# Optimization experiments

Hardware: AMD Instinct MI355X
Metric: run time of the kernel (lower is better)

## Reference

```python
import jax, jax.numpy as jnp
import numpy as np

N0 = 100000
N1 = 100000
K = 16
D_MODEL = 64
D_ATTN = 32
H = 4


def setup_inputs() -> dict:
    key = jax.random.key(0)
    ks = jax.random.split(key, 12)
    inp = {
        "coords0": jax.random.normal(ks[0], (N0, 3), jnp.float32),
        "coords1": jax.random.normal(ks[1], (N1, 3), jnp.float32),
        "feats0": jax.random.normal(ks[2], (N0, D_MODEL), jnp.float32),
        "feats1": jax.random.normal(ks[3], (N1, D_MODEL), jnp.float32),
        "knn_idxs": jax.random.randint(ks[4], (1, N1, K), 0, N0, jnp.int64 if jax.config.jax_enable_x64 else jnp.int32),
        # Linear params (PyTorch Linear: y = x @ W.T + b; stored here already transposed as [in, out])
        "Wq": jax.random.normal(ks[5], (D_MODEL, D_ATTN), jnp.float32) / np.sqrt(D_MODEL),
        "bq": jnp.zeros((D_ATTN,), jnp.float32),
        "Wk": jax.random.normal(ks[6], (D_MODEL + 3, D_ATTN), jnp.float32) / np.sqrt(D_MODEL + 3),
        "bk": jnp.zeros((D_ATTN,), jnp.float32),
        "Wv": jax.random.normal(ks[7], (D_MODEL + 3, D_MODEL), jnp.float32) / np.sqrt(D_MODEL + 3),
        "bv": jnp.zeros((D_MODEL,), jnp.float32),
    }
    return inp


def reference(coords0, coords1, feats0, feats1, knn_idxs, Wq, bq, Wk, bk, Wv, bv):
    idx = knn_idxs[0]  # [N1, K] neighbor indices into cloud 0
    n1, k_ = idx.shape
    dh_attn = D_ATTN // H   # per-head query/key depth
    dh_val = D_MODEL // H   # per-head value depth

    # Irregular gathers from source cloud
    g_feats = feats0[idx]                         # [N1, K, D_MODEL]
    rel = coords0[idx] - coords1[:, None, :]      # [N1, K, 3] relative coords
    kv_in = jnp.concatenate([g_feats, rel], axis=-1)  # [N1, K, D_MODEL+3]

    # Projections + head split
    q = (feats1 @ Wq + bq).reshape(n1, H, dh_attn)                    # [N1, H, dh]
    k = (kv_in @ Wk + bk).reshape(n1, k_, H, dh_attn).transpose(0, 2, 1, 3)  # [N1, H, K, dh]
    v = (kv_in @ Wv + bv).reshape(n1, k_, H, dh_val).transpose(0, 2, 1, 3)   # [N1, H, K, dv]

    # Attention over K neighbors per point
    attn = jnp.einsum('nhd,nhkd->nhk', q, k) / np.sqrt(dh_attn).astype(np.float32)
    attn = jax.nn.softmax(attn, axis=-1)          # [N1, H, K]
    out = jnp.einsum('nhk,nhkd->nhd', attn, v)    # [N1, H, dv]
    out = out.reshape(n1, -1)                     # [N1, D_MODEL]
    return out, knn_idxs
```

## Files before the change

kernel.cpp:

```cpp
#include <hip/hip_runtime.h>


using half8   = __attribute__((ext_vector_type(8))) _Float16;
using floatx4 = __attribute__((ext_vector_type(4))) float;

template<int CTRL>
__device__ __forceinline__ float dppAdd(float x) {
    int y = __builtin_amdgcn_update_dpp(0, __float_as_int(x), CTRL, 0xF, 0xF, true);
    return x + __int_as_float(y);
}
__device__ __forceinline__ float rowSum16(float x) {
    x = dppAdd<0x121>(x);
    x = dppAdd<0x122>(x);
    x = dppAdd<0x124>(x);
    x = dppAdd<0x128>(x);
    return x;
}

__global__ __launch_bounds__(256, 4) void proj_fused(
    const float* __restrict__ coords0,
    const float* __restrict__ feats0, const float* __restrict__ feats1,
    const float* __restrict__ Wq, const float* __restrict__ bq,
    const float* __restrict__ Wk, const float* __restrict__ bk,
    const float* __restrict__ Wv, const float* __restrict__ bv,
    _Float16* __restrict__ KVh, float* __restrict__ Qf,
    int n0, int n1, int nb0)
{
    __shared__ __align__(16) _Float16 sFrag[6144];
    __shared__ __align__(16) _Float16 sOut[6656];

    const int tid  = threadIdx.x;
    const int wave = tid >> 6;
    const int lane = tid & 63;
    const int l15  = lane & 15;
    const int quad = lane >> 4;

    if ((int)blockIdx.x < nb0) {
        const int rowBase = blockIdx.x * 64;
        for (int e = tid; e < 6144; e += 256) {
            int j = e & 7, ln = (e >> 3) & 63, h = (e >> 9) & 1, t = e >> 10;
            int k = h * 32 + ((ln >> 4) * 8) + j;
            int n = t * 16 + (ln & 15);
            float v = (n < 32) ? Wk[k * 32 + n] : Wv[k * 64 + (n - 32)];
            sFrag[e] = (_Float16)v;
        }
        __syncthreads();

        const int m0   = rowBase + wave * 16;
        const int row  = m0 + l15;
        const int rowc = (row < n0) ? row : (n0 - 1);
        const floatx4* X4 = (const floatx4*)(feats0 + (size_t)rowc * 64);
        floatx4 f0 = X4[quad * 2 + 0], f1 = X4[quad * 2 + 1];
        floatx4 f2 = X4[quad * 2 + 8], f3 = X4[quad * 2 + 9];
        half8 a0, a1;
        a0[0]=(_Float16)f0.x; a0[1]=(_Float16)f0.y; a0[2]=(_Float16)f0.z; a0[3]=(_Float16)f0.w;
        a0[4]=(_Float16)f1.x; a0[5]=(_Float16)f1.y; a0[6]=(_Float16)f1.z; a0[7]=(_Float16)f1.w;
        a1[0]=(_Float16)f2.x; a1[1]=(_Float16)f2.y; a1[2]=(_Float16)f2.z; a1[3]=(_Float16)f2.w;
        a1[4]=(_Float16)f3.x; a1[5]=(_Float16)f3.y; a1[6]=(_Float16)f3.z; a1[7]=(_Float16)f3.w;

        const half8* bf = (const half8*)sFrag;
        floatx4 acc[6];
        #pragma unroll
        for (int t = 0; t < 6; t++) {
            int n = t * 16 + l15;
            float bb = (n < 32) ? bk[n] : bv[n - 32];
            acc[t] = (floatx4){bb, bb, bb, bb};
        }
        #pragma unroll
        for (int t = 0; t < 6; t++) {
            acc[t] = __builtin_amdgcn_mfma_f32_16x16x32_f16(a0, bf[(t*2+0)*64 + lane], acc[t], 0,0,0);
            acc[t] = __builtin_amdgcn_mfma_f32_16x16x32_f16(a1, bf[(t*2+1)*64 + lane], acc[t], 0,0,0);
        }

        #pragma unroll
        for (int t = 0; t < 6; t++)
            #pragma unroll
            for (int r = 0; r < 4; r++)
                sOut[(wave * 16 + quad * 4 + r) * 104 + t * 16 + l15] = (_Float16)acc[t][r];

        for (int r2 = tid; r2 < 64; r2 += 256) {
            int rr = rowBase + r2;
            int rc = (rr < n0) ? rr : (n0 - 1);
            float* cw = (float*)(sOut + r2 * 104 + 96);
            cw[0] = coords0[(size_t)rc * 3 + 0];
            cw[1] = coords0[(size_t)rc * 3 + 1];
            cw[2] = coords0[(size_t)rc * 3 + 2];
            cw[3] = 0.f;
        }
        __syncthreads();

        const half8* so8 = (const half8*)sOut;
        half8* dst = (half8*)(KVh + (size_t)rowBase * 104);
        for (int c = tid; c < 832; c += 256) {
            int r = c / 13;
            if (rowBase + r < n0) dst[c] = so8[c];
        }
    } else {
        const int rowBase = ((int)blockIdx.x - nb0) * 64;
        for (int e = tid; e < 2048; e += 256) {
            int j = e & 7, ln = (e >> 3) & 63, h = (e >> 9) & 1, t = e >> 10;
            int k = h * 32 + ((ln >> 4) * 8) + j;
            int n = t * 16 + (ln & 15);
            sFrag[e] = (_Float16)Wq[k * 32 + n];
        }
        __syncthreads();

        const int m0   = rowBase + wave * 16;
        const int row  = m0 + l15;
        const int rowc = (row < n1) ? row : (n1 - 1);
        const floatx4* X4 = (const floatx4*)(feats1 + (size_t)rowc * 64);
        floatx4 f0 = X4[quad * 2 + 0], f1 = X4[quad * 2 + 1];
        floatx4 f2 = X4[quad * 2 + 8], f3 = X4[quad * 2 + 9];
        half8 a0, a1;
        a0[0]=(_Float16)f0.x; a0[1]=(_Float16)f0.y; a0[2]=(_Float16)f0.z; a0[3]=(_Float16)f0.w;
        a0[4]=(_Float16)f1.x; a0[5]=(_Float16)f1.y; a0[6]=(_Float16)f1.z; a0[7]=(_Float16)f1.w;
        a1[0]=(_Float16)f2.x; a1[1]=(_Float16)f2.y; a1[2]=(_Float16)f2.z; a1[3]=(_Float16)f2.w;
        a1[4]=(_Float16)f3.x; a1[5]=(_Float16)f3.y; a1[6]=(_Float16)f3.z; a1[7]=(_Float16)f3.w;

        const half8* bf = (const half8*)sFrag;
        floatx4 acc[2];
        #pragma unroll
        for (int t = 0; t < 2; t++) {
            float bb = bq[t * 16 + l15];
            acc[t] = (floatx4){bb, bb, bb, bb};
        }
        #pragma unroll
        for (int t = 0; t < 2; t++) {
            acc[t] = __builtin_amdgcn_mfma_f32_16x16x32_f16(a0, bf[(t*2+0)*64 + lane], acc[t], 0,0,0);
            acc[t] = __builtin_amdgcn_mfma_f32_16x16x32_f16(a1, bf[(t*2+1)*64 + lane], acc[t], 0,0,0);
        }
        #pragma unroll
        for (int t = 0; t < 2; t++)
            #pragma unroll
            for (int r = 0; r < 4; r++) {
                int ro = m0 + quad * 4 + r;
                if (ro < n1) Qf[(size_t)ro * 32 + t * 16 + l15] = acc[t][r];
            }
    }
}

__global__ __launch_bounds__(256, 4) void attn_kernel(
    const float* __restrict__ coords1,
    const int*   __restrict__ knn,
    const float* __restrict__ Qf, const _Float16* __restrict__ KVh,
    const float* __restrict__ Wk, const float* __restrict__ Wv,
    float* __restrict__ out, float* __restrict__ outIdx, int n1)
{
    __shared__ __align__(16) float sQ[16][36];
    __shared__ float sWk3[3][32];
    __shared__ float sWv3[3][64];
    __shared__ __align__(16) float sT[16][12];
    __shared__ __align__(16) int   sIdx[16][16];
    __shared__ __align__(16) float sA[16][68];

    const int tid = threadIdx.x;
    for (int e = tid; e < 288; e += 256) {
        if (e < 96) ((float*)sWk3)[e] = Wk[2048 + e];
        else        ((float*)sWv3)[e - 96] = Wv[4096 + (e - 96)];
    }
    if (tid < 128) {
        int pt = tid >> 3, c4 = tid & 7;
        int r = blockIdx.x * 16 + pt;
        if (r >= n1) r = n1 - 1;
        ((floatx4*)&sQ[pt][0])[c4] = ((const floatx4*)Qf)[(size_t)r * 8 + c4];
    }
    __syncthreads();

    const int p = tid >> 4;
    const int j = tid & 15;
    const int n = blockIdx.x * 16 + p;
    const bool valid = (n < n1);
    const int nc = valid ? n : (n1 - 1);

    const int idx = knn[nc * 16 + j];

    const half8* kr = (const half8*)(KVh + (size_t)idx * 104);
    half8 k8_0 = kr[0], k8_1 = kr[1], k8_2 = kr[2], k8_3 = kr[3];
    floatx4 cg = *(const floatx4*)(KVh + (size_t)idx * 104 + 96);

    const float r0 = cg[0] - coords1[nc * 3 + 0];
    const float r1 = cg[1] - coords1[nc * 3 + 1];
    const float r2 = cg[2] - coords1[nc * 3 + 2];

    const int g    = j & 7;
    const int hf   = j >> 3;
    const int h    = g >> 1;
    const int slot = ((j & 1) << 3) + (j >> 1);

    sIdx[p][slot] = idx;

    if (j < 12) {
        int c = j >> 2, h2 = j & 3;
        float t = 0.f;
        #pragma unroll
        for (int i = 0; i < 8; i++)
            t = fmaf(sWk3[c][h2 * 8 + i], sQ[p][h2 * 8 + i], t);
        sT[p][j] = t;
    }

    const int4* si4 = (const int4*)&sIdx[p][hf * 8];
    int4 viA = si4[0], viB = si4[1];
    int vIdx[8] = {viA.x, viA.y, viA.z, viA.w, viB.x, viB.y, viB.z, viB.w};
    half8 v8[8];
    #pragma unroll
    for (int s = 0; s < 8; s++)
        v8[s] = *(const half8*)(KVh + (size_t)vIdx[s] * 104 + 32 + g * 8);

    const floatx4* t4 = (const floatx4*)&sT[p][0];
    floatx4 tc0 = t4[0], tc1 = t4[1], tc2 = t4[2];

    const float scale = 0.35355339059327373f;
    float a_h[4];
    {
        half8 k8[4] = {k8_0, k8_1, k8_2, k8_3};
        #pragma unroll
        for (int h2 = 0; h2 < 4; h2++) {
            floatx4 q0 = ((const floatx4*)&sQ[p][0])[h2 * 2 + 0];
            floatx4 q1 = ((const floatx4*)&sQ[p][0])[h2 * 2 + 1];
            float acc = r0 * tc0[h2] + r1 * tc1[h2] + r2 * tc2[h2];
            acc = fmaf(q0[0], (float)k8[h2][0], acc);
            acc = fmaf(q0[1], (float)k8[h2][1], acc);
            acc = fmaf(q0[2], (float)k8[h2][2], acc);
            acc = fmaf(q0[3], (float)k8[h2][3], acc);
            acc = fmaf(q1[0], (float)k8[h2][4], acc);
            acc = fmaf(q1[1], (float)k8[h2][5], acc);
            acc = fmaf(q1[2], (float)k8[h2][6], acc);
            acc = fmaf(q1[3], (float)k8[h2][7], acc);
            float e = __expf(acc * scale);
            float ssum = rowSum16(e);
            a_h[h2] = e * __builtin_amdgcn_rcpf(ssum);
        }
    }

    sA[p][0 * 16 + slot] = a_h[0];
    sA[p][1 * 16 + slot] = a_h[1];
    sA[p][2 * 16 + slot] = a_h[2];
    sA[p][3 * 16 + slot] = a_h[3];

    if (valid) outIdx[n * 16 + j] = (float)idx;

    float rbs0, rbs1, rbs2;
    {
        float s00 = rowSum16(a_h[0] * r0), s01 = rowSum16(a_h[1] * r0);
        float s02 = rowSum16(a_h[2] * r0), s03 = rowSum16(a_h[3] * r0);
        rbs0 = (h == 0) ? s00 : (h == 1) ? s01 : (h == 2) ? s02 : s03;
        float s10 = rowSum16(a_h[0] * r1), s11 = rowSum16(a_h[1] * r1);
        float s12 = rowSum16(a_h[2] * r1), s13 = rowSum16(a_h[3] * r1);
        rbs1 = (h == 0) ? s10 : (h == 1) ? s11 : (h == 2) ? s12 : s13;
        float s20 = rowSum16(a_h[0] * r2), s21 = rowSum16(a_h[1] * r2);
        float s22 = rowSum16(a_h[2] * r2), s23 = rowSum16(a_h[3] * r2);
        rbs2 = (h == 0) ? s20 : (h == 1) ? s21 : (h == 2) ? s22 : s23;
    }

    const floatx4* a4 = (const floatx4*)&sA[p][h * 16 + hf * 8];
    floatx4 aw0 = a4[0], aw1 = a4[1];
    float av[8] = {aw0[0], aw0[1], aw0[2], aw0[3], aw1[0], aw1[1], aw1[2], aw1[3]};

    float acc8[8] = {0,0,0,0,0,0,0,0};
    #pragma unroll
    for (int s = 0; s < 8; s++)
        #pragma unroll
        for (int i = 0; i < 8; i++)
            acc8[i] = fmaf(av[s], (float)v8[s][i], acc8[i]);

    #pragma unroll
    for (int i = 0; i < 8; i++) acc8[i] = dppAdd<0x128>(acc8[i]);

    #pragma unroll
    for (int i = 0; i < 8; i++)
        acc8[i] += rbs0 * sWv3[0][8 * g + i] + rbs1 * sWv3[1][8 * g + i] + rbs2 * sWv3[2][8 * g + i];

    if (valid) {
        floatx4 st = { acc8[hf * 4 + 0], acc8[hf * 4 + 1], acc8[hf * 4 + 2], acc8[hf * 4 + 3] };
        ((floatx4*)out)[(size_t)n * 16 + g * 2 + hf] = st;
    }
}

extern "C" void kernel_launch(void* const* d_in, const int* in_sizes, int n_in,
                              void* d_out, int out_size, void* d_ws, size_t ws_size,
                              hipStream_t stream) {
    const float* coords0 = (const float*)d_in[0];
    const float* coords1 = (const float*)d_in[1];
    const float* feats0  = (const float*)d_in[2];
    const float* feats1  = (const float*)d_in[3];
    const int*   knn     = (const int*)d_in[4];
    const float* Wq      = (const float*)d_in[5];
    const float* bq      = (const float*)d_in[6];
    const float* Wk      = (const float*)d_in[7];
    const float* bk      = (const float*)d_in[8];
    const float* Wv      = (const float*)d_in[9];
    const float* bv      = (const float*)d_in[10];

    const int n0 = in_sizes[0] / 3;
    const int n1 = in_sizes[1] / 3;

    char* ws = (char*)d_ws;
    _Float16* KVh = (_Float16*)ws;
    float*    Qf  = (float*)(ws + (size_t)n0 * 104 * 2);

    float* out    = (float*)d_out;
    float* outIdx = out + (size_t)n1 * 64;

    const int nb0 = (n0 + 63) / 64;
    const int nb1 = (n1 + 63) / 64;

    proj_fused<<<nb0 + nb1, 256, 0, stream>>>(coords0, feats0, feats1,
                                              Wq, bq, Wk, bk, Wv, bv,
                                              KVh, Qf, n0, n1, nb0);
    attn_kernel<<<(n1 + 15) / 16, 256, 0, stream>>>(coords1, knn,
                                                    Qf, KVh, Wk, Wv, out, outIdx, n1);
}
```

Before: 207.0 us.

## Precompute fp16 weight fragments once and drop coords from KV rows

Adds a small prep kernel that converts Wq/Wk/Wv into fp16 MFMA fragment layout once per call. The projection blocks now copy that with vector loads instead of each block doing a scattered float gather and conversion. The KV row stride shrinks from 104 to 96 halves by no longer packing source coordinates into it. The attention kernel instead gathers coords0 directly by neighbor index, which adds three scalar gathers per neighbor in exchange for smaller KV writes and reads and one fewer kernel pass over coords.

```diff
diff --git a/kernel.cpp b/kernel.cpp
--- a/kernel.cpp
+++ b/kernel.cpp
@@ -17,17 +17,37 @@
     return x;
 }
 
+__global__ __launch_bounds__(256) void prep_weights(
+    const float* __restrict__ Wq, const float* __restrict__ Wk,
+    const float* __restrict__ Wv,
+    _Float16* __restrict__ fragKV, _Float16* __restrict__ fragQ)
+{
+    const int base = blockIdx.x * 256 + threadIdx.x;
+    for (int e = base; e < 6144; e += 2048) {
+        int j = e & 7, ln = (e >> 3) & 63, h = (e >> 9) & 1, t = e >> 10;
+        int k = h * 32 + ((ln >> 4) * 8) + j;
+        int n = t * 16 + (ln & 15);
+        float v = (n < 32) ? Wk[k * 32 + n] : Wv[k * 64 + (n - 32)];
+        fragKV[e] = (_Float16)v;
+    }
+    for (int e = base; e < 2048; e += 2048) {
+        int j = e & 7, ln = (e >> 3) & 63, h = (e >> 9) & 1, t = e >> 10;
+        int k = h * 32 + ((ln >> 4) * 8) + j;
+        int n = t * 16 + (ln & 15);
+        fragQ[e] = (_Float16)Wq[k * 32 + n];
+    }
+}
+
 __global__ __launch_bounds__(256, 4) void proj_fused(
-    const float* __restrict__ coords0,
     const float* __restrict__ feats0, const float* __restrict__ feats1,
-    const float* __restrict__ Wq, const float* __restrict__ bq,
-    const float* __restrict__ Wk, const float* __restrict__ bk,
-    const float* __restrict__ Wv, const float* __restrict__ bv,
+    const _Float16* __restrict__ fragKV, const _Float16* __restrict__ fragQ,
+    const float* __restrict__ bq, const float* __restrict__ bk,
+    const float* __restrict__ bv,
     _Float16* __restrict__ KVh, float* __restrict__ Qf,
     int n0, int n1, int nb0)
 {
     __shared__ __align__(16) _Float16 sFrag[6144];
-    __shared__ __align__(16) _Float16 sOut[6656];
+    __shared__ __align__(16) _Float16 sOut[6144];
 
     const int tid  = threadIdx.x;
     const int wave = tid >> 6;
@@ -37,13 +57,9 @@
 
     if ((int)blockIdx.x < nb0) {
         const int rowBase = blockIdx.x * 64;
-        for (int e = tid; e < 6144; e += 256) {
-            int j = e & 7, ln = (e >> 3) & 63, h = (e >> 9) & 1, t = e >> 10;
-            int k = h * 32 + ((ln >> 4) * 8) + j;
-            int n = t * 16 + (ln & 15);
-            float v = (n < 32) ? Wk[k * 32 + n] : Wv[k * 64 + (n - 32)];
-            sFrag[e] = (_Float16)v;
-        }
+        half8* sF8 = (half8*)sFrag;
+        const half8* fk8 = (const half8*)fragKV;
+        for (int c = tid; c < 768; c += 256) sF8[c] = fk8[c];
         __syncthreads();
 
         const int m0   = rowBase + wave * 16;
@@ -76,33 +92,20 @@
         for (int t = 0; t < 6; t++)
             #pragma unroll
             for (int r = 0; r < 4; r++)
-                sOut[(wave * 16 + quad * 4 + r) * 104 + t * 16 + l15] = (_Float16)acc[t][r];
-
-        for (int r2 = tid; r2 < 64; r2 += 256) {
-            int rr = rowBase + r2;
-            int rc = (rr < n0) ? rr : (n0 - 1);
-            float* cw = (float*)(sOut + r2 * 104 + 96);
-            cw[0] = coords0[(size_t)rc * 3 + 0];
-            cw[1] = coords0[(size_t)rc * 3 + 1];
-            cw[2] = coords0[(size_t)rc * 3 + 2];
-            cw[3] = 0.f;
-        }
+                sOut[(wave * 16 + quad * 4 + r) * 96 + t * 16 + l15] = (_Float16)acc[t][r];
         __syncthreads();
 
         const half8* so8 = (const half8*)sOut;
-        half8* dst = (half8*)(KVh + (size_t)rowBase * 104);
-        for (int c = tid; c < 832; c += 256) {
-            int r = c / 13;
+        half8* dst = (half8*)(KVh + (size_t)rowBase * 96);
+        for (int c = tid; c < 768; c += 256) {
+            int r = c / 12;
             if (rowBase + r < n0) dst[c] = so8[c];
         }
     } else {
         const int rowBase = ((int)blockIdx.x - nb0) * 64;
-        for (int e = tid; e < 2048; e += 256) {
-            int j = e & 7, ln = (e >> 3) & 63, h = (e >> 9) & 1, t = e >> 10;
-            int k = h * 32 + ((ln >> 4) * 8) + j;
-            int n = t * 16 + (ln & 15);
-            sFrag[e] = (_Float16)Wq[k * 32 + n];
-        }
+        half8* sF8 = (half8*)sFrag;
+        const half8* fq8 = (const half8*)fragQ;
+        for (int c = tid; c < 256; c += 256) sF8[c] = fq8[c];
         __syncthreads();
 
         const int m0   = rowBase + wave * 16;
@@ -140,7 +143,7 @@
 }
 
 __global__ __launch_bounds__(256, 4) void attn_kernel(
-    const float* __restrict__ coords1,
+    const float* __restrict__ coords0, const float* __restrict__ coords1,
     const int*   __restrict__ knn,
     const float* __restrict__ Qf, const _Float16* __restrict__ KVh,
     const float* __restrict__ Wk, const float* __restrict__ Wv,
@@ -174,13 +177,12 @@
 
     const int idx = knn[nc * 16 + j];
 
-    const half8* kr = (const half8*)(KVh + (size_t)idx * 104);
+    const half8* kr = (const half8*)(KVh + (size_t)idx * 96);
     half8 k8_0 = kr[0], k8_1 = kr[1], k8_2 = kr[2], k8_3 = kr[3];
-    floatx4 cg = *(const floatx4*)(KVh + (size_t)idx * 104 + 96);
-
-    const float r0 = cg[0] - coords1[nc * 3 + 0];
-    const float r1 = cg[1] - coords1[nc * 3 + 1];
-    const float r2 = cg[2] - coords1[nc * 3 + 2];
+
+    const float r0 = coords0[idx * 3 + 0] - coords1[nc * 3 + 0];
+    const float r1 = coords0[idx * 3 + 1] - coords1[nc * 3 + 1];
+    const float r2 = coords0[idx * 3 + 2] - coords1[nc * 3 + 2];
 
     const int g    = j & 7;
     const int hf   = j >> 3;
@@ -204,7 +206,7 @@
     half8 v8[8];
     #pragma unroll
     for (int s = 0; s < 8; s++)
-        v8[s] = *(const half8*)(KVh + (size_t)vIdx[s] * 104 + 32 + g * 8);
+        v8[s] = *(const half8*)(KVh + (size_t)vIdx[s] * 96 + 32 + g * 8);
 
     const floatx4* t4 = (const floatx4*)&sT[p][0];
     floatx4 tc0 = t4[0], tc1 = t4[1], tc2 = t4[2];
@@ -296,7 +298,9 @@
 
     char* ws = (char*)d_ws;
     _Float16* KVh = (_Float16*)ws;
-    float*    Qf  = (float*)(ws + (size_t)n0 * 104 * 2);
+    float*    Qf  = (float*)(ws + (size_t)n0 * 96 * 2);
+    _Float16* fragKV = (_Float16*)(ws + (size_t)n0 * 96 * 2 + (size_t)n1 * 32 * 4);
+    _Float16* fragQ  = fragKV + 6144;
 
     float* out    = (float*)d_out;
     float* outIdx = out + (size_t)n1 * 64;
@@ -304,9 +308,9 @@
     const int nb0 = (n0 + 63) / 64;
     const int nb1 = (n1 + 63) / 64;
 
-    proj_fused<<<nb0 + nb1, 256, 0, stream>>>(coords0, feats0, feats1,
-                                              Wq, bq, Wk, bk, Wv, bv,
-                                              KVh, Qf, n0, n1, nb0);
-    attn_kernel<<<(n1 + 15) / 16, 256, 0, stream>>>(coords1, knn,
+    prep_weights<<<8, 256, 0, stream>>>(Wq, Wk, Wv, fragKV, fragQ);
+    proj_fused<<<nb0 + nb1, 256, 0, stream>>>(feats0, feats1, fragKV, fragQ,
+                                              bq, bk, bv, KVh, Qf, n0, n1, nb0);
+    attn_kernel<<<(n1 + 15) / 16, 256, 0, stream>>>(coords0, coords1, knn,
                                                     Qf, KVh, Wk, Wv, out, outIdx, n1);
 }
```

Result: faster. 188.5 us (-9.0%).
